# Performance work log

Hardware: AMD Instinct MI355X
Metric: run time of the kernel (lower is better)

Reference implementation:

```python
import jax, jax.numpy as jnp
import numpy as np
from jax import lax

SCORE_TH = 0.05
IOU_TH = 0.5
MAX_DET = 100  # fixed keep budget per class (torch version is variable-length; we pad)
BBOX_STD = jnp.array([0.1, 0.1, 0.2, 0.2], dtype=jnp.float32)


def setup_inputs() -> dict:
    key = jax.random.key(0)
    k1, k2, k3, k4 = jax.random.split(key, 4)
    A, C, H, W = 200000, 80, 768, 768
    # sigmoid-like scores, skewed low so the 0.05 threshold is meaningful
    classification = jax.random.uniform(k1, (A, C), dtype=jnp.float32) ** 4
    regression = jax.random.normal(k2, (A, 4), dtype=jnp.float32)
    ctr = jax.random.uniform(k3, (A, 2), dtype=jnp.float32, minval=0.0, maxval=float(W))
    wh = jax.random.uniform(k4, (A, 2), dtype=jnp.float32, minval=8.0, maxval=128.0)
    anchors = jnp.concatenate([ctr - 0.5 * wh, ctr + 0.5 * wh], axis=-1)  # valid x1y1x2y2
    return {"classification": classification, "regression": regression,
            "anchors": anchors, "img_h": H, "img_w": W}


def _decode_clip(anchors, regression, img_h, img_w):
    # BBoxTransform: RetinaNet delta decode with std [0.1,0.1,0.2,0.2], then ClipBoxes
    wa = anchors[:, 2] - anchors[:, 0]
    ha = anchors[:, 3] - anchors[:, 1]
    cxa = anchors[:, 0] + 0.5 * wa
    cya = anchors[:, 1] + 0.5 * ha
    d = regression * BBOX_STD
    cx = cxa + d[:, 0] * wa
    cy = cya + d[:, 1] * ha
    w = jnp.exp(d[:, 2]) * wa
    h = jnp.exp(d[:, 3]) * ha
    boxes = jnp.stack([cx - 0.5 * w, cy - 0.5 * h, cx + 0.5 * w, cy + 0.5 * h], axis=-1)
    lim = jnp.array([img_w, img_h, img_w, img_h], dtype=boxes.dtype)
    return jnp.clip(boxes, 0.0, lim)


def _nms_one(scores_c, boxes, areas):
    # greedy NMS for one class over all A anchors; fixed MAX_DET iterations
    s0 = jnp.where(scores_c > SCORE_TH, scores_c, -1.0)

    def step(s, _):
        i = jnp.argmax(s)
        valid = s[i] > 0.0
        b = boxes[i]
        xx1 = jnp.maximum(b[0], boxes[:, 0])
        yy1 = jnp.maximum(b[1], boxes[:, 1])
        xx2 = jnp.minimum(b[2], boxes[:, 2])
        yy2 = jnp.minimum(b[3], boxes[:, 3])
        inter = jnp.maximum(xx2 - xx1, 0.0) * jnp.maximum(yy2 - yy1, 0.0)
        iou = inter / (areas[i] + areas - inter)
        supp = (iou > IOU_TH) & valid
        s = jnp.where(supp, -1.0, s).at[i].set(-1.0)
        return s, (i, valid)

    _, (idx, val) = lax.scan(step, s0, None, length=MAX_DET)
    return idx, val  # [MAX_DET] int, [MAX_DET] bool


def _forward(classification, regression, anchors, img_h, img_w):
    boxes = _decode_clip(anchors, regression, img_h, img_w)  # [A,4]
    # NMS index selection is non-differentiable (as in torch); stop_gradient the selection path
    boxes_ng = lax.stop_gradient(boxes)
    scores_ng = lax.stop_gradient(classification)
    areas = (boxes_ng[:, 2] - boxes_ng[:, 0]) * (boxes_ng[:, 3] - boxes_ng[:, 1])
    idx, val = jax.vmap(_nms_one, in_axes=(1, None, None))(scores_ng, boxes_ng, areas)  # [C,M]
    C = classification.shape[1]
    sel_scores = jnp.take_along_axis(classification.T, idx, axis=1) * val          # [C,M]
    sel_boxes = boxes[idx] * val[..., None]                                        # [C,M,4]
    class_ids = jnp.where(val, jnp.arange(C, dtype=jnp.int32)[:, None], -1)        # [C,M]
    # torch returns variable-length concatenations; we return fixed-size padded
    # equivalents (invalid slots: score=0, class=-1, box=0)
    return sel_scores.reshape(-1), class_ids.reshape(-1), sel_boxes.reshape(-1, 4)


def reference(classification, regression, anchors, img_h, img_w):
    return _forward(classification, regression, anchors, img_h, img_w)
```

## Files before the change

kernel.cpp:

```cpp
#include <hip/hip_runtime.h>
#include <float.h>
#include <math.h>

#define SCORE_TH 0.05f
#define IOU_TH   0.5f
#define MAXD     100
#define CAP      512
#define HI_TH    0.996f
#define SWALK    192
#define CNT_STRIDE 16

__device__ __forceinline__ float4 decode_box(float4 an, float4 r, float W, float H)
{
    float wa = an.z - an.x, ha = an.w - an.y;
    float cxa = an.x + 0.5f * wa, cya = an.y + 0.5f * ha;
    float cx = cxa + r.x * 0.1f * wa;
    float cy = cya + r.y * 0.1f * ha;
    float w  = expf(r.z * 0.2f) * wa;
    float h  = expf(r.w * 0.2f) * ha;
    float x1 = cx - 0.5f * w, y1 = cy - 0.5f * h;
    float x2 = cx + 0.5f * w, y2 = cy + 0.5f * h;
    x1 = fminf(fmaxf(x1, 0.f), W);
    y1 = fminf(fmaxf(y1, 0.f), H);
    x2 = fminf(fmaxf(x2, 0.f), W);
    y2 = fminf(fmaxf(y2, 0.f), H);
    return make_float4(x1, y1, x2, y2);
}

template<int CC>
__global__ __launch_bounds__(256)
void k_compact(const float4* __restrict__ cls4, float2* __restrict__ cand,
               int* __restrict__ cnt, int* __restrict__ loflag,
               int C_rt, int total4)
{
    const int C = CC ? CC : C_rt;
    __shared__ unsigned char lflag[256];
    for (int i = threadIdx.x; i < C; i += blockDim.x) lflag[i] = 0;
    __syncthreads();

    const int gstride = gridDim.x * blockDim.x;
    const int gtid = blockIdx.x * blockDim.x + threadIdx.x;

    for (int j0 = gtid; j0 < total4; j0 += 4 * gstride) {
        int j1 = j0 + gstride, j2 = j0 + 2 * gstride, j3 = j0 + 3 * gstride;
        bool ok1 = j1 < total4, ok2 = j2 < total4, ok3 = j3 < total4;
        float4 v0 = cls4[j0];
        float4 v1 = ok1 ? cls4[j1] : make_float4(0.f, 0.f, 0.f, 0.f);
        float4 v2 = ok2 ? cls4[j2] : make_float4(0.f, 0.f, 0.f, 0.f);
        float4 v3 = ok3 ? cls4[j3] : make_float4(0.f, 0.f, 0.f, 0.f);

        #pragma unroll
        for (int w = 0; w < 4; w++) {
            float4 v = (w == 0) ? v0 : (w == 1) ? v1 : (w == 2) ? v2 : v3;
            if (w == 1 && !ok1) break;
            if (w == 2 && !ok2) break;
            if (w == 3 && !ok3) break;
            unsigned b = (unsigned)(j0 + w * gstride) * 4u;
            int c = (int)(b % (unsigned)C);
            int a = (int)(b / (unsigned)C);
            float s[4] = {v.x, v.y, v.z, v.w};
            #pragma unroll
            for (int j = 0; j < 4; j++) {
                float sc = s[j];
                if (sc > HI_TH) {
                    int pos = atomicAdd(&cnt[c * CNT_STRIDE], 1);
                    if (pos < CAP) cand[(size_t)c * CAP + pos] = make_float2(sc, __int_as_float(a));
                } else if (sc > SCORE_TH) {
                    lflag[c] = 1;
                }
                c++; if (c == C) { c = 0; a++; }
            }
        }
    }
    __syncthreads();
    for (int i = threadIdx.x; i < C; i += blockDim.x)
        if (lflag[i]) loflag[i] = 1;
}

__global__ __launch_bounds__(256)
void k_nms(const float4* __restrict__ anch, const float4* __restrict__ reg,
           const int* __restrict__ ph, const int* __restrict__ pw,
           const float2* __restrict__ cand, const int* __restrict__ cnt,
           const int* __restrict__ loflag, int* __restrict__ incomp,
           float* __restrict__ out, int C)
{
    int c = blockIdx.x;
    __shared__ unsigned long long keys[CAP];
    __shared__ float bx1[SWALK], by1[SWALK], bx2[SWALK], by2[SWALK], sar[SWALK];
    __shared__ int   kidx[MAXD];
    __shared__ int   kept_s;

    int n_raw = cnt[c * CNT_STRIDE];
    if (n_raw > CAP) {
        if (threadIdx.x == 0) incomp[c] = 1;
        return;
    }
    int n = n_raw;

    for (int i = threadIdx.x; i < CAP; i += blockDim.x) {
        if (i < n) {
            float2 e = cand[(size_t)c * CAP + i];
            unsigned sbits = __float_as_uint(e.x);
            unsigned aid   = (unsigned)__float_as_int(e.y);
            keys[i] = ((unsigned long long)(~sbits) << 32) | (unsigned long long)aid;
        } else {
            keys[i] = 0xFFFFFFFFFFFFFFFFull;
        }
    }
    __syncthreads();

    const int SORTN = (n <= 256) ? 256 : CAP;
    for (int k = 2; k <= SORTN; k <<= 1) {
        for (int j = k >> 1; j > 0; j >>= 1) {
            for (int i = threadIdx.x; i < SORTN; i += blockDim.x) {
                int ixj = i ^ j;
                if (ixj > i) {
                    unsigned long long a = keys[i], b = keys[ixj];
                    bool sw = ((i & k) == 0) ? (a > b) : (a < b);
                    if (sw) { keys[i] = b; keys[ixj] = a; }
                }
            }
            __syncthreads();
        }
    }

    float W = (float)(*pw), H = (float)(*ph);
    int nS = n < SWALK ? n : SWALK;
    for (int i = threadIdx.x; i < nS; i += blockDim.x) {
        unsigned aid = (unsigned)keys[i];
        float4 b = decode_box(anch[aid], reg[aid], W, H);
        bx1[i] = b.x; by1[i] = b.y; bx2[i] = b.z; by2[i] = b.w;
        sar[i] = (b.z - b.x) * (b.w - b.y);
    }
    __syncthreads();

    if (threadIdx.x < 64) {
        int t = threadIdx.x;
        int kept = 0;
        float a0x1 = 0.f, a0y1 = 0.f, a0x2 = 0.f, a0y2 = 0.f, a0a = 0.f;
        float a1x1 = 0.f, a1y1 = 0.f, a1x2 = 0.f, a1y2 = 0.f, a1a = 0.f;
        for (int k = 0; k < nS && kept < MAXD; ++k) {
            float cx1 = bx1[k], cy1 = by1[k], cx2 = bx2[k], cy2 = by2[k], ca = sar[k];
            bool supp = false;
            if (t < kept) {
                float xx1 = fmaxf(cx1, a0x1), yy1 = fmaxf(cy1, a0y1);
                float xx2 = fminf(cx2, a0x2), yy2 = fminf(cy2, a0y2);
                float inter = fmaxf(xx2 - xx1, 0.f) * fmaxf(yy2 - yy1, 0.f);
                float iou = inter / (ca + a0a - inter);
                supp = iou > IOU_TH;
            }
            if (64 + t < kept) {
                float xx1 = fmaxf(cx1, a1x1), yy1 = fmaxf(cy1, a1y1);
                float xx2 = fminf(cx2, a1x2), yy2 = fminf(cy2, a1y2);
                float inter = fmaxf(xx2 - xx1, 0.f) * fmaxf(yy2 - yy1, 0.f);
                float iou = inter / (ca + a1a - inter);
                supp = supp || (iou > IOU_TH);
            }
            if (!__any(supp)) {
                if (kept == t)            { a0x1 = cx1; a0y1 = cy1; a0x2 = cx2; a0y2 = cy2; a0a = ca; }
                else if (kept == 64 + t)  { a1x1 = cx1; a1y1 = cy1; a1x2 = cx2; a1y2 = cy2; a1a = ca; }
                if (t == 0) kidx[kept] = k;
                ++kept;
            }
        }
        if (t == 0) kept_s = kept;
    }
    __syncthreads();

    int kept = kept_s;
    if (kept < MAXD && (n > nS || loflag[c] != 0)) {
        if (threadIdx.x == 0) incomp[c] = 1;
        return;
    }

    int total = C * MAXD;
    int base = c * MAXD;
    for (int m = threadIdx.x; m < kept; m += blockDim.x) {
        int k = kidx[m];
        unsigned long long key = keys[k];
        float sc = __uint_as_float(~(unsigned)(key >> 32));
        out[base + m] = sc;
        out[total + base + m] = (float)c;
        float* ob = out + 2 * (size_t)total + (size_t)(base + m) * 4;
        ob[0] = bx1[k]; ob[1] = by1[k]; ob[2] = bx2[k]; ob[3] = by2[k];
    }
    for (int m = kept + threadIdx.x; m < MAXD; m += blockDim.x) {
        out[base + m] = 0.f;
        out[total + base + m] = -1.f;
        float* ob = out + 2 * (size_t)total + (size_t)(base + m) * 4;
        ob[0] = 0.f; ob[1] = 0.f; ob[2] = 0.f; ob[3] = 0.f;
    }
}

__global__ __launch_bounds__(256)
void k_fallback(const float* __restrict__ cls,
                const float4* __restrict__ anch, const float4* __restrict__ reg,
                const int* __restrict__ ph, const int* __restrict__ pw,
                const int* __restrict__ incomp, float* __restrict__ out,
                int A, int C)
{
    int c = blockIdx.x;
    if (!incomp[c]) return;
    __shared__ float kx1[MAXD], ky1[MAXD], kx2[MAXD], ky2[MAXD], kar[MAXD];
    __shared__ float rs[4]; __shared__ int ra[4];
    __shared__ float cs; __shared__ int caid; __shared__ int have; __shared__ int suppflag;
    int lane = threadIdx.x & 63, wid = threadIdx.x >> 6;
    float W = (float)(*pw), H = (float)(*ph);
    float s_last = FLT_MAX; int a_last = -1;
    int kept = 0;
    int total = C * MAXD;
    for (long long guard = 0; guard <= (long long)A && kept < MAXD; guard++) {
        float bs = -1.f; int ba = 0x7fffffff;
        for (int a = threadIdx.x; a < A; a += blockDim.x) {
            float s = cls[(size_t)a * C + c];
            if (s <= SCORE_TH) continue;
            if (s > s_last || (s == s_last && a <= a_last)) continue;
            if (s > bs || (s == bs && a < ba)) { bs = s; ba = a; }
        }
        for (int off = 32; off >= 1; off >>= 1) {
            float s2 = __shfl_down(bs, off);
            int a2 = __shfl_down(ba, off);
            if (s2 > bs || (s2 == bs && a2 < ba)) { bs = s2; ba = a2; }
        }
        if (lane == 0) { rs[wid] = bs; ra[wid] = ba; }
        __syncthreads();
        if (threadIdx.x == 0) {
            float fs = rs[0]; int fa = ra[0];
            for (int w = 1; w < 4; w++)
                if (rs[w] > fs || (rs[w] == fs && ra[w] < fa)) { fs = rs[w]; fa = ra[w]; }
            cs = fs; caid = fa; have = (fs > 0.f) ? 1 : 0;
        }
        __syncthreads();
        if (!have) break;
        float s_c = cs; int a_c = caid;
        s_last = s_c; a_last = a_c;
        float4 b = decode_box(anch[a_c], reg[a_c], W, H);
        float ar = (b.z - b.x) * (b.w - b.y);
        if (threadIdx.x == 0) suppflag = 0;
        __syncthreads();
        for (int k = threadIdx.x; k < kept; k += blockDim.x) {
            float xx1 = fmaxf(b.x, kx1[k]);
            float yy1 = fmaxf(b.y, ky1[k]);
            float xx2 = fminf(b.z, kx2[k]);
            float yy2 = fminf(b.w, ky2[k]);
            float inter = fmaxf(xx2 - xx1, 0.f) * fmaxf(yy2 - yy1, 0.f);
            float iou = inter / (ar + kar[k] - inter);
            if (iou > IOU_TH) suppflag = 1;
        }
        __syncthreads();
        if (!suppflag) {
            if (threadIdx.x == 0) {
                kx1[kept] = b.x; ky1[kept] = b.y; kx2[kept] = b.z; ky2[kept] = b.w; kar[kept] = ar;
                int slot = c * MAXD + kept;
                out[slot] = s_c;
                out[total + slot] = (float)c;
                float* ob = out + 2 * (size_t)total + (size_t)slot * 4;
                ob[0] = b.x; ob[1] = b.y; ob[2] = b.z; ob[3] = b.w;
            }
            kept++;
        }
        __syncthreads();
    }
    for (int k = kept + threadIdx.x; k < MAXD; k += blockDim.x) {
        int slot = c * MAXD + k;
        out[slot] = 0.f;
        out[total + slot] = -1.f;
        float* ob = out + 2 * (size_t)total + (size_t)slot * 4;
        ob[0] = 0.f; ob[1] = 0.f; ob[2] = 0.f; ob[3] = 0.f;
    }
}

extern "C" void kernel_launch(void* const* d_in, const int* in_sizes, int n_in,
                              void* d_out, int out_size, void* d_ws, size_t ws_size,
                              hipStream_t stream)
{
    const float*  cls  = (const float*)d_in[0];
    const float4* reg  = (const float4*)d_in[1];
    const float4* anch = (const float4*)d_in[2];
    const int*    ph   = (const int*)d_in[3];
    const int*    pw   = (const int*)d_in[4];
    int A = in_sizes[1] / 4;
    int C = in_sizes[0] / A;
    float* out = (float*)d_out;

    char* ws = (char*)d_ws;
    float2* cand = (float2*)ws;
    int* ctrl   = (int*)(cand + (size_t)C * CAP);
    int* cnt    = ctrl;
    int* loflag = ctrl + C * CNT_STRIDE;
    int* incomp = loflag + C;

    hipMemsetAsync(ctrl, 0, (C * CNT_STRIDE + 2 * C) * sizeof(int), stream);

    int total4 = (int)((long long)A * C / 4);
    int blocks2 = (total4 + 255) / 256;
    if (blocks2 > 2048) blocks2 = 2048;
    if (C == 80 && (long long)A * C < (1LL << 31))
        k_compact<80><<<blocks2, 256, 0, stream>>>((const float4*)cls, cand, cnt, loflag, C, total4);
    else
        k_compact<0><<<blocks2, 256, 0, stream>>>((const float4*)cls, cand, cnt, loflag, C, total4);

    k_nms<<<C, 256, 0, stream>>>(anch, reg, ph, pw, cand, cnt, loflag, incomp, out, C);
    k_fallback<<<C, 256, 0, stream>>>(cls, anch, reg, ph, pw, incomp, out, A, C);
}
```

Measured before the change: 144.7 us.

## Replace serial greedy NMS walk with parallel IoU bitmask and redundant scan

Instead of a single wavefront walking candidates and testing each one against the kept boxes with a ballot, all threads first compute a pairwise suppression bitmask over the top SWALK candidates (three 64-bit words per row). Every thread then scans the mask sequentially to pick kept boxes, so no broadcast or ballot is needed. This spreads the IoU work over the whole block and shortens the serial dependency chain. In exchange it computes up to nS²/2 IoUs instead of only those against kept boxes, and adds about 4.6KB of shared memory.

Measured after the change: 145.9 us. About the same (+0.8%).

```diff
diff --git a/kernel.cpp b/kernel.cpp
--- a/kernel.cpp
+++ b/kernel.cpp
@@ -8,6 +8,7 @@
 #define CAP      512
 #define HI_TH    0.996f
 #define SWALK    192
+#define NWORDS   3
 #define CNT_STRIDE 16
 
 __device__ __forceinline__ float4 decode_box(float4 an, float4 r, float W, float H)
@@ -87,8 +88,8 @@
     int c = blockIdx.x;
     __shared__ unsigned long long keys[CAP];
     __shared__ float bx1[SWALK], by1[SWALK], bx2[SWALK], by2[SWALK], sar[SWALK];
-    __shared__ int   kidx[MAXD];
-    __shared__ int   kept_s;
+    __shared__ unsigned long long mask[SWALK][NWORDS];
+    __shared__ int kidx[MAXD];
 
     int n_raw = cnt[c * CNT_STRIDE];
     if (n_raw > CAP) {
@@ -134,40 +135,40 @@
     }
     __syncthreads();
 
-    if (threadIdx.x < 64) {
-        int t = threadIdx.x;
-        int kept = 0;
-        float a0x1 = 0.f, a0y1 = 0.f, a0x2 = 0.f, a0y2 = 0.f, a0a = 0.f;
-        float a1x1 = 0.f, a1y1 = 0.f, a1x2 = 0.f, a1y2 = 0.f, a1a = 0.f;
-        for (int k = 0; k < nS && kept < MAXD; ++k) {
-            float cx1 = bx1[k], cy1 = by1[k], cx2 = bx2[k], cy2 = by2[k], ca = sar[k];
-            bool supp = false;
-            if (t < kept) {
-                float xx1 = fmaxf(cx1, a0x1), yy1 = fmaxf(cy1, a0y1);
-                float xx2 = fminf(cx2, a0x2), yy2 = fminf(cy2, a0y2);
-                float inter = fmaxf(xx2 - xx1, 0.f) * fmaxf(yy2 - yy1, 0.f);
-                float iou = inter / (ca + a0a - inter);
-                supp = iou > IOU_TH;
-            }
-            if (64 + t < kept) {
-                float xx1 = fmaxf(cx1, a1x1), yy1 = fmaxf(cy1, a1y1);
-                float xx2 = fminf(cx2, a1x2), yy2 = fminf(cy2, a1y2);
-                float inter = fmaxf(xx2 - xx1, 0.f) * fmaxf(yy2 - yy1, 0.f);
-                float iou = inter / (ca + a1a - inter);
-                supp = supp || (iou > IOU_TH);
-            }
-            if (!__any(supp)) {
-                if (kept == t)            { a0x1 = cx1; a0y1 = cy1; a0x2 = cx2; a0y2 = cy2; a0a = ca; }
-                else if (kept == 64 + t)  { a1x1 = cx1; a1y1 = cy1; a1x2 = cx2; a1y2 = cy2; a1a = ca; }
-                if (t == 0) kidx[kept] = k;
-                ++kept;
-            }
-        }
-        if (t == 0) kept_s = kept;
-    }
-    __syncthreads();
-
-    int kept = kept_s;
+    for (int task = threadIdx.x; task < nS * NWORDS; task += blockDim.x) {
+        int i = task / NWORDS;
+        int w = task - i * NWORDS;
+        unsigned long long m = 0ull;
+        int j0 = w << 6;
+        int jend = j0 + 64 < nS ? j0 + 64 : nS;
+        int js = j0 > i + 1 ? j0 : i + 1;
+        float ix1 = bx1[i], iy1 = by1[i], ix2 = bx2[i], iy2 = by2[i], ia = sar[i];
+        for (int j = js; j < jend; ++j) {
+            float xx1 = fmaxf(ix1, bx1[j]);
+            float yy1 = fmaxf(iy1, by1[j]);
+            float xx2 = fminf(ix2, bx2[j]);
+            float yy2 = fminf(iy2, by2[j]);
+            float inter = fmaxf(xx2 - xx1, 0.f) * fmaxf(yy2 - yy1, 0.f);
+            float iou = inter / (ia + sar[j] - inter);
+            if (iou > IOU_TH) m |= 1ull << (j - j0);
+        }
+        mask[i][w] = m;
+    }
+    __syncthreads();
+
+    unsigned long long rem0 = 0, rem1 = 0, rem2 = 0;
+    int kept = 0;
+    for (int k = 0; k < nS && kept < MAXD; ++k) {
+        unsigned long long m0 = mask[k][0], m1 = mask[k][1], m2 = mask[k][2];
+        unsigned long long rw = (k < 64) ? rem0 : (k < 128) ? rem1 : rem2;
+        if (!((rw >> (k & 63)) & 1ull)) {
+            if (threadIdx.x == 0) kidx[kept] = k;
+            ++kept;
+            rem0 |= m0; rem1 |= m1; rem2 |= m2;
+        }
+    }
+    __syncthreads();
+
     if (kept < MAXD && (n > nS || loflag[c] != 0)) {
         if (threadIdx.x == 0) incomp[c] = 1;
         return;
```
